# Optimization experiments

Measured on AMD Instinct MI355X. Metric: run time of the kernel, lower is better.

## Reference

```python
import jax, jax.numpy as jnp
import numpy as np

B, S, D = 16, 2048, 768  # batch, padded subword length, roberta hidden dim


def setup_inputs() -> dict:
    key = jax.random.key(0)
    k1, k2 = jax.random.split(key)
    robert_embed = jax.random.normal(k1, (B, S, D), dtype=jnp.float32)
    # Non-decreasing per-row segment ids: contiguous runs of equal ids are the
    # subword spans that merge_list would average; singleton runs pass through.
    seg_ids = jnp.sort(jax.random.randint(k2, (B, S), 0, S, dtype=jnp.int32), axis=-1)
    return {"robert_embed": robert_embed, "seg_ids": seg_ids}


def reference(robert_embed, seg_ids):
    # Segment-mean gather/scatter: out[b, w] = mean_{p: seg_ids[b,p]==w} x[b, p]
    b, s, d = robert_embed.shape
    w = s  # output word slots (<= s); empty slots yield zeros
    flat_seg = (seg_ids + (w * jnp.arange(b, dtype=seg_ids.dtype))[:, None]).reshape(-1)
    x_flat = robert_embed.reshape(-1, d)
    sums = jax.ops.segment_sum(x_flat, flat_seg, num_segments=b * w)  # [b*w, d]
    counts = jax.ops.segment_sum(
        jnp.ones((b * s,), dtype=robert_embed.dtype), flat_seg, num_segments=b * w
    )
    out = sums / jnp.maximum(counts, 1)[:, None]
    return out.reshape(b, w, d)
```

## Files before the change

### kernel.cpp

```cpp
#include <hip/hip_runtime.h>

#define BB 16
#define SS 2048
#define DD 768
#define D4 (DD / 4)
#define CH 8

__global__ __launch_bounds__(256) void seg_mean_stream(
    const float* __restrict__ x,
    const int*   __restrict__ seg,
    float*       __restrict__ out) {
    int lane = threadIdx.x & 63;
    int wave = threadIdx.x >> 6;
    int gw   = (blockIdx.x << 2) + wave;
    int p0   = gw * CH;
    int b    = p0 >> 11;
    int q0   = p0 & (SS - 1);
    const int*   srow = seg + (b << 11);
    const float* xb   = x   + (size_t)(b << 11) * DD;
    float*       ob   = out + (size_t)(b << 11) * DD;

    bool startl = false;
    if (lane < CH) {
        int p   = q0 + lane;
        int myv = srow[p];
        int pv  = (p == 0) ? (myv ^ 1) : srow[p - 1];
        startl  = (myv != pv);
    }
    unsigned long long smask = __ballot(startl);

    const float4 zz = make_float4(0.f, 0.f, 0.f, 0.f);

    if (q0 == 0) {
        int first = srow[0];
        for (int z = 0; z < first; ++z) {
            float4* zp = (float4*)(ob + (size_t)z * DD);
            zp[lane] = zz; zp[lane + 64] = zz; zp[lane + 128] = zz;
        }
    }

    while (smask) {
        int i = (int)__builtin_ctzll(smask);
        smask &= smask - 1;
        int s = q0 + i;
        int v = srow[s];
        int e;
        if (smask) {
            e = q0 + (int)__builtin_ctzll(smask);
        } else {
            e = q0 + CH;
            for (;;) {
                int idx = e + lane;
                int vv  = (idx < SS) ? srow[idx] : (v ^ 1);
                unsigned long long m  = __ballot(vv == v);
                unsigned long long nm = ~m;
                if (nm) { e += (int)__builtin_ctzll(nm); break; }
                e += 64;
            }
        }
        int c     = e - s;
        int vnext = (e < SS) ? srow[e] : SS;

        const float4* xp = (const float4*)(xb + (size_t)s * DD);
        float4 a0 = xp[lane];
        float4 a1 = xp[lane + 64];
        float4 a2 = xp[lane + 128];
        if (c > 1) {
            const float4* xr = xp + D4;
            float4 r0 = xr[lane], r1 = xr[lane + 64], r2 = xr[lane + 128];
            for (int j = 2; j < c; ++j) {
                const float4* xn = xp + (size_t)j * D4;
                float4 t0 = xn[lane], t1 = xn[lane + 64], t2 = xn[lane + 128];
                a0.x += r0.x; a0.y += r0.y; a0.z += r0.z; a0.w += r0.w;
                a1.x += r1.x; a1.y += r1.y; a1.z += r1.z; a1.w += r1.w;
                a2.x += r2.x; a2.y += r2.y; a2.z += r2.z; a2.w += r2.w;
                r0 = t0; r1 = t1; r2 = t2;
            }
            a0.x += r0.x; a0.y += r0.y; a0.z += r0.z; a0.w += r0.w;
            a1.x += r1.x; a1.y += r1.y; a1.z += r1.z; a1.w += r1.w;
            a2.x += r2.x; a2.y += r2.y; a2.z += r2.z; a2.w += r2.w;
        }
        float inv = 1.0f / (float)c;
        a0.x *= inv; a0.y *= inv; a0.z *= inv; a0.w *= inv;
        a1.x *= inv; a1.y *= inv; a1.z *= inv; a1.w *= inv;
        a2.x *= inv; a2.y *= inv; a2.z *= inv; a2.w *= inv;

        float4* op = (float4*)(ob + (size_t)v * DD);
        op[lane] = a0; op[lane + 64] = a1; op[lane + 128] = a2;

        for (int z = v + 1; z < vnext; ++z) {
            float4* zp = (float4*)(ob + (size_t)z * DD);
            zp[lane] = zz; zp[lane + 64] = zz; zp[lane + 128] = zz;
        }
    }
}

extern "C" void kernel_launch(void* const* d_in, const int* in_sizes, int n_in,
                              void* d_out, int out_size, void* d_ws, size_t ws_size,
                              hipStream_t stream) {
    const float* x   = (const float*)d_in[0];
    const int*   seg = (const int*)d_in[1];
    float* out = (float*)d_out;

    int nBlocks = (BB * SS) / (4 * CH);
    seg_mean_stream<<<nBlocks, 256, 0, stream>>>(x, seg, out);
}
```

Before: 185.4 us.

## Prefetch chunk rows into registers up front and use nontemporal output stores

Each wave now loads all eight of its chunk's rows into registers before scanning the segment ids, so that load latency overlaps with the boundary detection. Segments are then accumulated in an unrolled pass over those registers, and only the run spilling past the chunk reads extra rows. Output and zero-fill writes use nontemporal stores to avoid polluting cache, and launch bounds request higher occupancy. The trade-off is heavy register pressure from 24 float4 values per lane, which could cause spills or reduce occupancy.

```diff
diff --git a/kernel.cpp b/kernel.cpp
--- a/kernel.cpp
+++ b/kernel.cpp
@@ -6,7 +6,36 @@
 #define D4 (DD / 4)
 #define CH 8
 
-__global__ __launch_bounds__(256) void seg_mean_stream(
+#define ADD4(A, R) { A.x += R.x; A.y += R.y; A.z += R.z; A.w += R.w; }
+
+typedef __attribute__((ext_vector_type(4))) float f32x4;
+
+__device__ __forceinline__ void nt_store(float4 v, float4* p) {
+    f32x4 t; t.x = v.x; t.y = v.y; t.z = v.z; t.w = v.w;
+    __builtin_nontemporal_store(t, (f32x4*)p);
+}
+
+__device__ __forceinline__ void emit_row(float* __restrict__ ob, int v, int vnext,
+                                         int c, float4 a0, float4 a1, float4 a2,
+                                         int lane) {
+    float inv = 1.0f / (float)c;
+    a0.x *= inv; a0.y *= inv; a0.z *= inv; a0.w *= inv;
+    a1.x *= inv; a1.y *= inv; a1.z *= inv; a1.w *= inv;
+    a2.x *= inv; a2.y *= inv; a2.z *= inv; a2.w *= inv;
+    float4* op = (float4*)(ob + (size_t)v * DD);
+    nt_store(a0, op + lane);
+    nt_store(a1, op + lane + 64);
+    nt_store(a2, op + lane + 128);
+    const float4 zz = make_float4(0.f, 0.f, 0.f, 0.f);
+    for (int z = v + 1; z < vnext; ++z) {
+        float4* zp = (float4*)(ob + (size_t)z * DD);
+        nt_store(zz, zp + lane);
+        nt_store(zz, zp + lane + 64);
+        nt_store(zz, zp + lane + 128);
+    }
+}
+
+__global__ __launch_bounds__(256, 4) void seg_mean_v4(
     const float* __restrict__ x,
     const int*   __restrict__ seg,
     float*       __restrict__ out) {
@@ -20,79 +49,77 @@
     const float* xb   = x   + (size_t)(b << 11) * DD;
     float*       ob   = out + (size_t)(b << 11) * DD;
 
+    float4 r[CH][3];
+    #pragma unroll
+    for (int j = 0; j < CH; ++j) {
+        const float4* xp = (const float4*)(xb + (size_t)(q0 + j) * DD);
+        r[j][0] = xp[lane];
+        r[j][1] = xp[lane + 64];
+        r[j][2] = xp[lane + 128];
+    }
+
+    int  myv = 0;
     bool startl = false;
     if (lane < CH) {
-        int p   = q0 + lane;
-        int myv = srow[p];
-        int pv  = (p == 0) ? (myv ^ 1) : srow[p - 1];
-        startl  = (myv != pv);
+        int p = q0 + lane;
+        myv = srow[p];
+        int pv = (p == 0) ? (myv ^ 1) : srow[p - 1];
+        startl = (myv != pv);
     }
     unsigned long long smask = __ballot(startl);
 
-    const float4 zz = make_float4(0.f, 0.f, 0.f, 0.f);
-
     if (q0 == 0) {
         int first = srow[0];
+        const float4 zz = make_float4(0.f, 0.f, 0.f, 0.f);
         for (int z = 0; z < first; ++z) {
             float4* zp = (float4*)(ob + (size_t)z * DD);
-            zp[lane] = zz; zp[lane + 64] = zz; zp[lane + 128] = zz;
+            nt_store(zz, zp + lane);
+            nt_store(zz, zp + lane + 64);
+            nt_store(zz, zp + lane + 128);
+        }
+    }
+    if (!smask) return;
+
+    int i0 = (int)__builtin_ctzll(smask);
+
+    float4 a0 = make_float4(0.f,0.f,0.f,0.f), a1 = a0, a2 = a0;
+    int s_rel = 0, vcur = 0;
+    #pragma unroll
+    for (int j = 0; j < CH; ++j) {
+        if (j >= i0) {
+            if ((smask >> j) & 1) {
+                s_rel = j;
+                vcur  = __shfl(myv, j);
+                a0 = r[j][0]; a1 = r[j][1]; a2 = r[j][2];
+            } else {
+                ADD4(a0, r[j][0]); ADD4(a1, r[j][1]); ADD4(a2, r[j][2]);
+            }
+            if (j + 1 < CH && ((smask >> (j + 1)) & 1)) {
+                int vnext = __shfl(myv, j + 1);
+                emit_row(ob, vcur, vnext, j + 1 - s_rel, a0, a1, a2, lane);
+            }
         }
     }
 
-    while (smask) {
-        int i = (int)__builtin_ctzll(smask);
-        smask &= smask - 1;
-        int s = q0 + i;
-        int v = srow[s];
-        int e;
-        if (smask) {
-            e = q0 + (int)__builtin_ctzll(smask);
-        } else {
-            e = q0 + CH;
-            for (;;) {
-                int idx = e + lane;
-                int vv  = (idx < SS) ? srow[idx] : (v ^ 1);
-                unsigned long long m  = __ballot(vv == v);
-                unsigned long long nm = ~m;
-                if (nm) { e += (int)__builtin_ctzll(nm); break; }
-                e += 64;
-            }
-        }
-        int c     = e - s;
-        int vnext = (e < SS) ? srow[e] : SS;
-
-        const float4* xp = (const float4*)(xb + (size_t)s * DD);
-        float4 a0 = xp[lane];
-        float4 a1 = xp[lane + 64];
-        float4 a2 = xp[lane + 128];
-        if (c > 1) {
-            const float4* xr = xp + D4;
-            float4 r0 = xr[lane], r1 = xr[lane + 64], r2 = xr[lane + 128];
-            for (int j = 2; j < c; ++j) {
-                const float4* xn = xp + (size_t)j * D4;
-                float4 t0 = xn[lane], t1 = xn[lane + 64], t2 = xn[lane + 128];
-                a0.x += r0.x; a0.y += r0.y; a0.z += r0.z; a0.w += r0.w;
-                a1.x += r1.x; a1.y += r1.y; a1.z += r1.z; a1.w += r1.w;
-                a2.x += r2.x; a2.y += r2.y; a2.z += r2.z; a2.w += r2.w;
-                r0 = t0; r1 = t1; r2 = t2;
-            }
-            a0.x += r0.x; a0.y += r0.y; a0.z += r0.z; a0.w += r0.w;
-            a1.x += r1.x; a1.y += r1.y; a1.z += r1.z; a1.w += r1.w;
-            a2.x += r2.x; a2.y += r2.y; a2.z += r2.z; a2.w += r2.w;
-        }
-        float inv = 1.0f / (float)c;
-        a0.x *= inv; a0.y *= inv; a0.z *= inv; a0.w *= inv;
-        a1.x *= inv; a1.y *= inv; a1.z *= inv; a1.w *= inv;
-        a2.x *= inv; a2.y *= inv; a2.z *= inv; a2.w *= inv;
-
-        float4* op = (float4*)(ob + (size_t)v * DD);
-        op[lane] = a0; op[lane + 64] = a1; op[lane + 128] = a2;
-
-        for (int z = v + 1; z < vnext; ++z) {
-            float4* zp = (float4*)(ob + (size_t)z * DD);
-            zp[lane] = zz; zp[lane + 64] = zz; zp[lane + 128] = zz;
+    int ilast = 63 - (int)__builtin_clzll(smask);
+    int e = q0 + CH;
+    if (e < SS) {
+        for (;;) {
+            int idx = e + lane;
+            int vv  = (idx < SS) ? srow[idx] : (vcur ^ 1);
+            unsigned long long m  = __ballot(vv == vcur);
+            unsigned long long nm = ~m;
+            if (nm) { e += (int)__builtin_ctzll(nm); break; }
+            e += 64;
         }
     }
+    for (int t = q0 + CH; t < e; ++t) {
+        const float4* xn = (const float4*)(xb + (size_t)t * DD);
+        float4 t0 = xn[lane], t1 = xn[lane + 64], t2 = xn[lane + 128];
+        ADD4(a0, t0); ADD4(a1, t1); ADD4(a2, t2);
+    }
+    int vnext = (e < SS) ? srow[e] : SS;
+    emit_row(ob, vcur, vnext, e - (q0 + ilast), a0, a1, a2, lane);
 }
 
 extern "C" void kernel_launch(void* const* d_in, const int* in_sizes, int n_in,
@@ -103,5 +130,5 @@
     float* out = (float*)d_out;
 
     int nBlocks = (BB * SS) / (4 * CH);
-    seg_mean_stream<<<nBlocks, 256, 0, stream>>>(x, seg, out);
+    seg_mean_v4<<<nBlocks, 256, 0, stream>>>(x, seg, out);
 }
```

Result: faster. 180.3 us (-2.7%).
